# Performance work log

Hardware: AMD Instinct MI355X
Metric: run time of the kernel (lower is better)

Reference implementation:

```python
import jax, jax.numpy as jnp
import numpy as np

B, T, E, H = 2, 2048, 1024, 16


def setup_inputs() -> dict:
    key = jax.random.key(0)
    ks = jax.random.split(key, 6)
    s = lambda k, shape: jax.random.normal(k, shape, dtype=jnp.float32) * 0.02
    return {
        "x": jax.random.normal(ks[0], (B, T, E), dtype=jnp.float32),
        "ln1_g": jnp.ones((E,), jnp.float32),
        "ln1_b": jnp.zeros((E,), jnp.float32),
        "attn_w": s(ks[1], (E, 3 * E)),
        "attn_b": jnp.zeros((3 * E,), jnp.float32),
        "proj_w": s(ks[2], (E, E)),
        "proj_b": jnp.zeros((E,), jnp.float32),
        "ln2_g": jnp.ones((E,), jnp.float32),
        "ln2_b": jnp.zeros((E,), jnp.float32),
        "mlp_w1": s(ks[3], (E, 4 * E)),
        "mlp_b1": jnp.zeros((4 * E,), jnp.float32),
        "mlp_w2": s(ks[4], (4 * E, E)),
        "mlp_b2": jnp.zeros((E,), jnp.float32),
        "w_att": jnp.ones((1,), jnp.float32),
        "w_mlp": jnp.ones((1,), jnp.float32),
    }


def _ln(x, g, b, eps=1e-5):
    m = x.mean(-1, keepdims=True)
    v = ((x - m) ** 2).mean(-1, keepdims=True)
    return (x - m) * jax.lax.rsqrt(v + eps) * g + b


def reference(x, ln1_g, ln1_b, attn_w, attn_b, proj_w, proj_b,
              ln2_g, ln2_b, mlp_w1, mlp_b1, mlp_w2, mlp_b2, w_att, w_mlp):
    Bx, Tx, Ex = x.shape
    hd = Ex // H
    # --- self-attention on ln_1(x) ---
    qkv = _ln(x, ln1_g, ln1_b) @ attn_w + attn_b          # [B,T,3E]
    q, k, v = jnp.split(qkv, 3, axis=-1)
    q = q.reshape(Bx, Tx, H, hd)
    k = k.reshape(Bx, Tx, H, hd)
    v = v.reshape(Bx, Tx, H, hd)
    att = jnp.einsum('bthd,bshd->bhts', q, k) * (1.0 / np.sqrt(hd))  # [B,H,T,T]
    causal = jnp.tril(jnp.ones((Tx, Tx), dtype=bool))
    att = jnp.where(causal, att, -jnp.inf)
    att = jax.nn.softmax(att, axis=-1)
    y = jnp.einsum('bhts,bshd->bthd', att, v).reshape(Bx, Tx, Ex)
    y = y @ proj_w + proj_b
    x = x * w_att + y
    # --- MLP on ln_2(x) ---
    h = _ln(x, ln2_g, ln2_b) @ mlp_w1 + mlp_b1
    h = jax.nn.gelu(h, approximate=False)
    x = x * w_mlp + (h @ mlp_w2 + mlp_b2)
    return x
```

## Files before the change

### kernel.cpp

```cpp
#include <hip/hip_runtime.h>
#include <math.h>

typedef __bf16 bf16;
typedef bf16 bf16x8 __attribute__((ext_vector_type(8)));
typedef bf16 bf16x4 __attribute__((ext_vector_type(4)));
typedef float f32x4 __attribute__((ext_vector_type(4)));

#define MFMA(a, b, c) __builtin_amdgcn_mfma_f32_16x16x32_bf16((a), (b), (c), 0, 0, 0)

#define GLOAD_LDS16(gp, lp)                                                        \
  __builtin_amdgcn_global_load_lds((const __attribute__((address_space(1))) void*)(gp), \
                                   (__attribute__((address_space(3))) void*)(lp), 16, 0, 0)

static const size_t E_WT_ATTN = 0;
static const size_t E_WT_PROJ = 3145728;
static const size_t E_WT_MLP1 = 4194304;
static const size_t E_WT_MLP2 = 8388608;
static const size_t E_LN1     = 12582912;
static const size_t E_QKV     = 16777216;
static const size_t E_VT      = 37748736;
static const size_t E_Y       = 41943040;
static const size_t E_LN2     = 46137344;
static const size_t E_H       = 50331648;
static const size_t BYTE_X2    = 134217728;
static const size_t BYTE_OPART = 150994944;
static const size_t BYTE_ML    = 184549376;
static const size_t BYTE_GPART = 185597952;
static const size_t TOTAL_BYTES = 252706816;

__device__ __align__(4096) unsigned char g_buf[TOTAL_BYTES];

__global__ __launch_bounds__(256) void transpose_cast(const float* __restrict__ in,
                                                      bf16* __restrict__ out, int K, int N) {
  __shared__ float tile[32][33];
  int bx = blockIdx.x, by = blockIdx.y;
  int tx = threadIdx.x, ty = threadIdx.y;
#pragma unroll
  for (int i = ty; i < 32; i += 8)
    tile[i][tx] = in[(size_t)(by * 32 + i) * N + bx * 32 + tx];
  __syncthreads();
#pragma unroll
  for (int i = ty; i < 32; i += 8)
    out[(size_t)(bx * 32 + i) * K + by * 32 + tx] = (bf16)tile[tx][i];
}

__global__ __launch_bounds__(256) void ln_bf16(const float* __restrict__ x,
                                               const float* __restrict__ g,
                                               const float* __restrict__ b,
                                               bf16* __restrict__ out) {
  int row = blockIdx.x, tid = threadIdx.x;
  const float* xr = x + ((size_t)row << 10);
  float4 v = *(const float4*)(xr + tid * 4);
  float s = v.x + v.y + v.z + v.w;
  float ss = v.x * v.x + v.y * v.y + v.z * v.z + v.w * v.w;
#pragma unroll
  for (int off = 32; off >= 1; off >>= 1) {
    s += __shfl_down(s, off);
    ss += __shfl_down(ss, off);
  }
  __shared__ float sh[8];
  int wid = tid >> 6;
  if ((tid & 63) == 0) { sh[wid] = s; sh[wid + 4] = ss; }
  __syncthreads();
  float ts = sh[0] + sh[1] + sh[2] + sh[3];
  float tss = sh[4] + sh[5] + sh[6] + sh[7];
  float mean = ts * (1.0f / 1024.0f);
  float var = tss * (1.0f / 1024.0f) - mean * mean;
  float inv = rsqrtf(var + 1e-5f);
  float4 gg = *(const float4*)(g + tid * 4);
  float4 bb = *(const float4*)(b + tid * 4);
  bf16x4 o;
  o[0] = (bf16)((v.x - mean) * inv * gg.x + bb.x);
  o[1] = (bf16)((v.y - mean) * inv * gg.y + bb.y);
  o[2] = (bf16)((v.z - mean) * inv * gg.z + bb.z);
  o[3] = (bf16)((v.w - mean) * inv * gg.w + bb.w);
  *(bf16x4*)(out + ((size_t)row << 10) + tid * 4) = o;
}

template <int EPI>
__global__ __launch_bounds__(512, 2) void gemm256(const bf16* __restrict__ A,
                                                  const bf16* __restrict__ Bt,
                                                  const float* __restrict__ bias,
                                                  bf16* __restrict__ outb,
                                                  float* __restrict__ outf,
                                                  int M, int N, int K, int Kseg) {
  __shared__ __align__(16) bf16 As[2][16384];
  __shared__ __align__(16) bf16 Bs[2][16384];
  int tid = threadIdx.x;
  int nwg = gridDim.x * gridDim.y;
  int bid = blockIdx.y * gridDim.x + blockIdx.x;
  int id2 = ((nwg & 7) == 0) ? ((bid & 7) * (nwg >> 3) + (bid >> 3)) : bid;
  int bx = id2 % gridDim.x, by = id2 / gridDim.x;
  int lane = tid & 63, wid = tid >> 6;
  int wr = wid >> 2, wc = wid & 3;
  int g = lane >> 4, lr = lane & 15;
  f32x4 acc[8][4];
#pragma unroll
  for (int m = 0; m < 8; ++m)
#pragma unroll
    for (int n = 0; n < 4; ++n) acc[m][n] = (f32x4){0.f, 0.f, 0.f, 0.f};
  const bf16* Ab = A + (size_t)by * 256 * K;
  const bf16* Bb = Bt + (size_t)bx * 256 * K;
  int rbase = tid >> 3;
  int srccol = (((tid & 7) ^ (rbase & 7)) << 3);
  const bf16* Asrc = Ab + (size_t)rbase * K + srccol;
  const bf16* Bsrc = Bb + (size_t)rbase * K + srccol;
#define G256_STAGE(buf, k0)                                                \
  {                                                                        \
    _Pragma("unroll") for (int q = 0; q < 4; ++q) {                        \
      GLOAD_LDS16(Asrc + (size_t)(q * 64) * K + (k0), &As[buf][tid * 8 + q * 4096]); \
      GLOAD_LDS16(Bsrc + (size_t)(q * 64) * K + (k0), &Bs[buf][tid * 8 + q * 4096]); \
    }                                                                      \
  }
  int kbeg = blockIdx.z * Kseg;
  int NT = Kseg >> 6;
  G256_STAGE(0, kbeg);
  __syncthreads();
  int c = 0;
  for (int t = 0; t < NT; ++t) {
    if (t + 1 < NT) G256_STAGE(c ^ 1, kbeg + (t + 1) * 64);
#pragma unroll
    for (int kk = 0; kk < 2; ++kk) {
      bf16x8 af[8], bfv[4];
#pragma unroll
      for (int m = 0; m < 8; ++m) {
        int row = wr * 128 + m * 16 + lr;
        af[m] = *(const bf16x8*)&As[c][row * 64 + ((((kk << 2) + g) ^ (row & 7)) << 3)];
      }
#pragma unroll
      for (int n = 0; n < 4; ++n) {
        int row = wc * 64 + n * 16 + lr;
        bfv[n] = *(const bf16x8*)&Bs[c][row * 64 + ((((kk << 2) + g) ^ (row & 7)) << 3)];
      }
#pragma unroll
      for (int m = 0; m < 8; ++m)
#pragma unroll
        for (int n = 0; n < 4; ++n) acc[m][n] = MFMA(af[m], bfv[n], acc[m][n]);
    }
    __syncthreads();
    c ^= 1;
  }
#undef G256_STAGE
  if (EPI == 3) {
    float* po = outf + (size_t)blockIdx.z * M * N;
#pragma unroll
    for (int m = 0; m < 8; ++m) {
#pragma unroll
      for (int n = 0; n < 4; ++n) {
        int rg0 = by * 256 + wr * 128 + m * 16 + g * 4;
        int cg = bx * 256 + wc * 64 + n * 16 + lr;
#pragma unroll
        for (int j = 0; j < 4; ++j) po[(size_t)(rg0 + j) * N + cg] = acc[m][n][j];
      }
    }
  } else {
#pragma unroll
    for (int m = 0; m < 8; ++m) {
#pragma unroll
      for (int n = 0; n < 4; ++n) {
        int rg0 = by * 256 + wr * 128 + m * 16 + g * 4;
        int cg = bx * 256 + wc * 64 + n * 16 + lr;
        float bv = bias[cg];
#pragma unroll
        for (int j = 0; j < 4; ++j) {
          float v = acc[m][n][j] + bv;
          size_t idx = (size_t)(rg0 + j) * N + cg;
          if (EPI == 0)
            outb[idx] = (bf16)v;
          else
            outb[idx] = (bf16)(0.5f * v * (1.0f + erff(v * 0.70710678118f)));
        }
      }
    }
  }
}

__global__ __launch_bounds__(256) void gemm_bt3(const bf16* __restrict__ A,
                                                const bf16* __restrict__ Bt,
                                                float* __restrict__ outf,
                                                int M, int N, int K, int Kseg) {
  __shared__ __align__(16) bf16 As[128 * 32];
  __shared__ __align__(16) bf16 Bs[128 * 32];
  int bx = blockIdx.x, by = blockIdx.y;
  int tid = threadIdx.x;
  int lane = tid & 63, wid = tid >> 6;
  int wr = wid >> 1, wc = wid & 1;
  int g = lane >> 4, lr = lane & 15;
  f32x4 acc[4][4];
#pragma unroll
  for (int m = 0; m < 4; ++m)
#pragma unroll
    for (int n = 0; n < 4; ++n) acc[m][n] = (f32x4){0.f, 0.f, 0.f, 0.f};
  const bf16* Ab = A + (size_t)by * 128 * K;
  const bf16* Bb = Bt + (size_t)bx * 128 * K;
  int srow = tid >> 2;
  int sk8 = (tid & 3) * 8;
  const bf16* Ap0 = Ab + (size_t)srow * K + sk8;
  const bf16* Ap1 = Ab + (size_t)(srow + 64) * K + sk8;
  const bf16* Bp0 = Bb + (size_t)srow * K + sk8;
  const bf16* Bp1 = Bb + (size_t)(srow + 64) * K + sk8;
  bf16* lA0 = As + tid * 8;
  bf16* lA1 = As + 2048 + tid * 8;
  bf16* lB0 = Bs + tid * 8;
  bf16* lB1 = Bs + 2048 + tid * 8;
  int kbeg = blockIdx.z * Kseg;
  int kend = kbeg + Kseg;
  for (int k0 = kbeg; k0 < kend; k0 += 32) {
    GLOAD_LDS16(Ap0 + k0, lA0);
    GLOAD_LDS16(Ap1 + k0, lA1);
    GLOAD_LDS16(Bp0 + k0, lB0);
    GLOAD_LDS16(Bp1 + k0, lB1);
    __syncthreads();
    bf16x8 af[4], bfv[4];
#pragma unroll
    for (int m = 0; m < 4; ++m) af[m] = *(const bf16x8*)(As + (wr * 64 + m * 16 + lr) * 32 + g * 8);
#pragma unroll
    for (int n = 0; n < 4; ++n) bfv[n] = *(const bf16x8*)(Bs + (wc * 64 + n * 16 + lr) * 32 + g * 8);
#pragma unroll
    for (int m = 0; m < 4; ++m)
#pragma unroll
      for (int n = 0; n < 4; ++n) acc[m][n] = MFMA(af[m], bfv[n], acc[m][n]);
    __syncthreads();
  }
  float* po = outf + (size_t)blockIdx.z * M * N;
#pragma unroll
  for (int m = 0; m < 4; ++m) {
#pragma unroll
    for (int n = 0; n < 4; ++n) {
      int rg0 = by * 128 + wr * 64 + m * 16 + g * 4;
      int cg = bx * 128 + wc * 64 + n * 16 + lr;
#pragma unroll
      for (int j = 0; j < 4; ++j) po[(size_t)(rg0 + j) * N + cg] = acc[m][n][j];
    }
  }
}

template <int SK>
__global__ __launch_bounds__(256) void reduce_add(const float* __restrict__ part,
                                                  const float* __restrict__ bias,
                                                  const float* __restrict__ res,
                                                  const float* __restrict__ wsc,
                                                  float* __restrict__ out, int MN, int N) {
  size_t i = ((size_t)blockIdx.x * 256 + threadIdx.x) * 4;
  float4 a = *(const float4*)(part + i);
#pragma unroll
  for (int s = 1; s < SK; ++s) {
    float4 b = *(const float4*)(part + (size_t)s * MN + i);
    a.x += b.x; a.y += b.y; a.z += b.z; a.w += b.w;
  }
  int col = (int)(i & (size_t)(N - 1));
  float4 bv = *(const float4*)(bias + col);
  float4 rv = *(const float4*)(res + i);
  float w = wsc[0];
  float4 o;
  o.x = rv.x * w + a.x + bv.x;
  o.y = rv.y * w + a.y + bv.y;
  o.z = rv.z * w + a.z + bv.z;
  o.w = rv.w * w + a.w + bv.w;
  *(float4*)(out + i) = o;
}

__global__ __launch_bounds__(256) void reduce_ln(const float* __restrict__ part,
                                                 const float* __restrict__ bias,
                                                 const float* __restrict__ res,
                                                 const float* __restrict__ wsc,
                                                 const float* __restrict__ lng,
                                                 const float* __restrict__ lnb,
                                                 float* __restrict__ x2out,
                                                 bf16* __restrict__ lnout) {
  int row = blockIdx.x, tid = threadIdx.x;
  size_t i = ((size_t)row << 10) + tid * 4;
  float4 a = *(const float4*)(part + i);
  float4 b2 = *(const float4*)(part + 4194304 + i);
  float4 rv = *(const float4*)(res + i);
  float4 bv = *(const float4*)(bias + tid * 4);
  float w = wsc[0];
  float4 o;
  o.x = rv.x * w + a.x + b2.x + bv.x;
  o.y = rv.y * w + a.y + b2.y + bv.y;
  o.z = rv.z * w + a.z + b2.z + bv.z;
  o.w = rv.w * w + a.w + b2.w + bv.w;
  *(float4*)(x2out + i) = o;
  float s = o.x + o.y + o.z + o.w;
  float ss = o.x * o.x + o.y * o.y + o.z * o.z + o.w * o.w;
#pragma unroll
  for (int off = 32; off >= 1; off >>= 1) {
    s += __shfl_down(s, off);
    ss += __shfl_down(ss, off);
  }
  __shared__ float sh[8];
  int wid = tid >> 6;
  if ((tid & 63) == 0) { sh[wid] = s; sh[wid + 4] = ss; }
  __syncthreads();
  float ts = sh[0] + sh[1] + sh[2] + sh[3];
  float tss = sh[4] + sh[5] + sh[6] + sh[7];
  float mean = ts * (1.0f / 1024.0f);
  float var = tss * (1.0f / 1024.0f) - mean * mean;
  float inv = rsqrtf(var + 1e-5f);
  float4 gg = *(const float4*)(lng + tid * 4);
  float4 bb = *(const float4*)(lnb + tid * 4);
  bf16x4 ov;
  ov[0] = (bf16)((o.x - mean) * inv * gg.x + bb.x);
  ov[1] = (bf16)((o.y - mean) * inv * gg.y + bb.y);
  ov[2] = (bf16)((o.z - mean) * inv * gg.z + bb.z);
  ov[3] = (bf16)((o.w - mean) * inv * gg.w + bb.w);
  *(bf16x4*)(lnout + ((size_t)row << 10) + tid * 4) = ov;
}

__global__ __launch_bounds__(256) void split_v_t(const bf16* __restrict__ qkv,
                                                 bf16* __restrict__ vT) {
  int t0 = blockIdx.x * 32;
  int bh = blockIdx.y;
  int b = bh >> 4, h = bh & 15;
  __shared__ bf16 tile[32][72];
  int tid = threadIdx.x;
  int d = tid & 63, tl0 = tid >> 6;
#pragma unroll
  for (int p = 0; p < 8; ++p) {
    int tl = p * 4 + tl0;
    tile[tl][d] = qkv[((size_t)(b * 2048 + t0 + tl)) * 3072 + 2048 + h * 64 + d];
  }
  __syncthreads();
  int tl = tid & 31, dq = tid >> 5;
#pragma unroll
  for (int p = 0; p < 8; ++p) {
    int dd = p * 8 + dq;
    vT[((size_t)(bh * 64 + dd)) * 2048 + t0 + tl] = tile[tl][dd];
  }
}

__global__ __launch_bounds__(256) void attn_fwd(const bf16* __restrict__ qkv,
                                                const bf16* __restrict__ vT,
                                                float* __restrict__ o_part,
                                                float* __restrict__ ml_part) {
  __shared__ __align__(16) bf16 Ks[2][4096];
  __shared__ __align__(16) bf16 Vs[2][4096];
  __shared__ bf16 P[4][16][72];
  int id = blockIdx.x;
  int bh = id & 31;
  int seg = (id >> 5) & 1;
  int qi = ((id >> 6) + bh) & 31;
  int tid = threadIdx.x, wid = tid >> 6, lane = tid & 63;
  int g = lane >> 4, lr = lane & 15;
  int b = bh >> 4, h = bh & 15;
  int nk = qi + 1;
  int n0 = (nk + 1) >> 1;
  int kt0 = seg ? n0 : 0;
  int kt1 = seg ? nk : n0;
  int qrow = qi * 64 + wid * 16 + lr;
  const bf16* Qr = qkv + ((size_t)(b * 2048 + qrow)) * 3072 + h * 64;
  bf16x8 qf[2];
  qf[0] = *(const bf16x8*)(Qr + g * 8);
  qf[1] = *(const bf16x8*)(Qr + 32 + g * 8);
  int r0 = tid >> 3, cs0 = ((tid & 7) ^ (r0 & 7)) << 3;
  int c1i = tid + 256;
  int r1 = c1i >> 3, cs1 = ((c1i & 7) ^ (r1 & 7)) << 3;
  const bf16* sK0 = qkv + ((size_t)(b * 2048 + r0)) * 3072 + 1024 + h * 64 + cs0;
  const bf16* sK1 = qkv + ((size_t)(b * 2048 + r1)) * 3072 + 1024 + h * 64 + cs1;
  const bf16* sV0 = vT + (size_t)bh * 131072 + (size_t)r0 * 2048 + cs0;
  const bf16* sV1 = vT + (size_t)bh * 131072 + (size_t)r1 * 2048 + cs1;
  bf16* dK0 = &Ks[0][0] + tid * 8;
  bf16* dK1 = &Ks[0][0] + 2048 + tid * 8;
  bf16* dV0 = &Vs[0][0] + tid * 8;
  bf16* dV1 = &Vs[0][0] + 2048 + tid * 8;
#define ATTN_STAGE(bufsel, ktv)                          \
  {                                                      \
    size_t kadv = (size_t)(ktv) * (64 * 3072);           \
    size_t vadv = (size_t)(ktv) * 64;                    \
    int bo = (bufsel) * 4096;                            \
    GLOAD_LDS16(sK0 + kadv, dK0 + bo);                   \
    GLOAD_LDS16(sK1 + kadv, dK1 + bo);                   \
    GLOAD_LDS16(sV0 + vadv, dV0 + bo);                   \
    GLOAD_LDS16(sV1 + vadv, dV1 + bo);                   \
  }
  f32x4 o[4];
#pragma unroll
  for (int n = 0; n < 4; ++n) o[n] = (f32x4){0.f, 0.f, 0.f, 0.f};
  float m = -3e38f, l = 0.f;
  if (kt0 < kt1) ATTN_STAGE(0, kt0);
  __syncthreads();
  const float beta = 0.18033688f;
  int sw = lr & 7;
  int sb = (lane & 48) | (g << 2);
  for (int kt = kt0; kt < kt1; ++kt) {
    int cur = (kt - kt0) & 1;
    if (kt + 1 < kt1) ATTN_STAGE(cur ^ 1, kt + 1);
    const bf16* Kb = &Ks[cur][0];
    const bf16* Vb = &Vs[cur][0];
    f32x4 s[4];
#pragma unroll
    for (int n = 0; n < 4; ++n) s[n] = (f32x4){0.f, 0.f, 0.f, 0.f};
#pragma unroll
    for (int kk = 0; kk < 2; ++kk) {
#pragma unroll
      for (int n = 0; n < 4; ++n) {
        bf16x8 kf = *(const bf16x8*)(Kb + ((n * 16 + lr) << 6) + ((((kk << 2) + g) ^ sw) << 3));
        s[n] = MFMA(kf, qf[kk], s[n]);
      }
    }
    int kc0 = kt * 64 + g * 4;
#pragma unroll
    for (int n = 0; n < 4; ++n)
#pragma unroll
      for (int j = 0; j < 4; ++j) {
        float sv = s[n][j] * beta;
        s[n][j] = ((kc0 + n * 16 + j) <= qrow) ? sv : -3e38f;
      }
    float mx = s[0][0];
#pragma unroll
    for (int n = 0; n < 4; ++n)
#pragma unroll
      for (int j = 0; j < 4; ++j) mx = fmaxf(mx, s[n][j]);
    mx = fmaxf(mx, __shfl_xor(mx, 16));
    mx = fmaxf(mx, __shfl_xor(mx, 32));
    float mn = fmaxf(m, mx);
    float al = exp2f(m - mn);
    m = mn;
    float rs = 0.f;
    bf16x4 pw[4];
#pragma unroll
    for (int n = 0; n < 4; ++n)
#pragma unroll
      for (int j = 0; j < 4; ++j) {
        float p = exp2f(s[n][j] - mn);
        rs += p;
        pw[n][j] = (bf16)p;
      }
    rs += __shfl_xor(rs, 16);
    rs += __shfl_xor(rs, 32);
    l = l * al + rs;
    float alj[4];
#pragma unroll
    for (int j = 0; j < 4; ++j) alj[j] = __shfl(al, sb + j);
#pragma unroll
    for (int n = 0; n < 4; ++n)
#pragma unroll
      for (int j = 0; j < 4; ++j) o[n][j] *= alj[j];
#pragma unroll
    for (int n = 0; n < 4; ++n) *(bf16x4*)&P[wid][lr][n * 16 + g * 4] = pw[n];
#pragma unroll
    for (int kk = 0; kk < 2; ++kk) {
      bf16x8 pf = *(const bf16x8*)&P[wid][lr][kk * 32 + g * 8];
#pragma unroll
      for (int n = 0; n < 4; ++n) {
        bf16x8 vf = *(const bf16x8*)(Vb + ((n * 16 + lr) << 6) + ((((kk << 2) + g) ^ sw) << 3));
        o[n] = MFMA(pf, vf, o[n]);
      }
    }
    __syncthreads();
  }
  float* ob = o_part + (size_t)id * 4096;
#pragma unroll
  for (int n = 0; n < 4; ++n)
#pragma unroll
    for (int j = 0; j < 4; ++j)
      ob[(size_t)(wid * 16 + g * 4 + j) * 64 + n * 16 + lr] = o[n][j];
  if (lane < 16) {
    ml_part[(size_t)id * 128 + (wid * 16 + lane) * 2] = m;
    ml_part[(size_t)id * 128 + (wid * 16 + lane) * 2 + 1] = l;
  }
#undef ATTN_STAGE
}

__global__ __launch_bounds__(256) void attn_combine(const float* __restrict__ o_part,
                                                    const float* __restrict__ ml_part,
                                                    bf16* __restrict__ y) {
  int c = blockIdx.x;
  int bh = c & 31, qi = c >> 5;
  int b = bh >> 4, h = bh & 15;
  int qraw = (qi - bh) & 31;
  size_t id0 = (size_t)bh + ((size_t)qraw << 6);
  size_t id1 = id0 + 32;
  int t = threadIdx.x;
  int r = t >> 2, cq = (t & 3) << 4;
  float m1 = ml_part[id0 * 128 + r * 2], l1 = ml_part[id0 * 128 + r * 2 + 1];
  float m2 = ml_part[id1 * 128 + r * 2], l2 = ml_part[id1 * 128 + r * 2 + 1];
  float mm = fmaxf(m1, m2);
  float w1 = exp2f(m1 - mm), w2 = exp2f(m2 - mm);
  float inv = 1.0f / (l1 * w1 + l2 * w2);
  const float* p1 = o_part + id0 * 4096 + r * 64 + cq;
  const float* p2 = o_part + id1 * 4096 + r * 64 + cq;
  bf16* yp = y + ((size_t)(b * 2048 + qi * 64 + r)) * 1024 + h * 64 + cq;
#pragma unroll
  for (int u = 0; u < 4; ++u) {
    float4 a = *(const float4*)(p1 + u * 4);
    float4 bq = *(const float4*)(p2 + u * 4);
    bf16x4 ov;
    ov[0] = (bf16)((a.x * w1 + bq.x * w2) * inv);
    ov[1] = (bf16)((a.y * w1 + bq.y * w2) * inv);
    ov[2] = (bf16)((a.z * w1 + bq.z * w2) * inv);
    ov[3] = (bf16)((a.w * w1 + bq.w * w2) * inv);
    *(bf16x4*)(yp + u * 4) = ov;
  }
}

extern "C" void kernel_launch(void* const* d_in, const int* in_sizes, int n_in,
                              void* d_out, int out_size, void* d_ws, size_t ws_size,
                              hipStream_t stream) {
  const float* x = (const float*)d_in[0];
  const float* ln1_g = (const float*)d_in[1];
  const float* ln1_b = (const float*)d_in[2];
  const float* attn_w = (const float*)d_in[3];
  const float* attn_b = (const float*)d_in[4];
  const float* proj_w = (const float*)d_in[5];
  const float* proj_b = (const float*)d_in[6];
  const float* ln2_g = (const float*)d_in[7];
  const float* ln2_b = (const float*)d_in[8];
  const float* mlp_w1 = (const float*)d_in[9];
  const float* mlp_b1 = (const float*)d_in[10];
  const float* mlp_w2 = (const float*)d_in[11];
  const float* mlp_b2 = (const float*)d_in[12];
  const float* w_att = (const float*)d_in[13];
  const float* w_mlp = (const float*)d_in[14];
  float* out = (float*)d_out;

  unsigned char* base = nullptr;
  if (ws_size >= TOTAL_BYTES) {
    base = (unsigned char*)d_ws;
  } else {
    hipGetSymbolAddress((void**)&base, HIP_SYMBOL(g_buf));
  }
  bf16* bb = (bf16*)base;
  bf16* wt_attn = bb + E_WT_ATTN;
  bf16* wt_proj = bb + E_WT_PROJ;
  bf16* wt_mlp1 = bb + E_WT_MLP1;
  bf16* wt_mlp2 = bb + E_WT_MLP2;
  bf16* ln1o = bb + E_LN1;
  bf16* qkv = bb + E_QKV;
  bf16* vTb = bb + E_VT;
  bf16* yb = bb + E_Y;
  bf16* ln2o = bb + E_LN2;
  bf16* hb = bb + E_H;
  float* x2 = (float*)(base + BYTE_X2);
  float* o_part = (float*)(base + BYTE_OPART);
  float* ml_part = (float*)(base + BYTE_ML);
  float* gpart = (float*)(base + BYTE_GPART);

  dim3 tb(32, 8);
  transpose_cast<<<dim3(3072 / 32, 1024 / 32), tb, 0, stream>>>(attn_w, wt_attn, 1024, 3072);
  transpose_cast<<<dim3(1024 / 32, 1024 / 32), tb, 0, stream>>>(proj_w, wt_proj, 1024, 1024);
  transpose_cast<<<dim3(4096 / 32, 1024 / 32), tb, 0, stream>>>(mlp_w1, wt_mlp1, 1024, 4096);
  transpose_cast<<<dim3(1024 / 32, 4096 / 32), tb, 0, stream>>>(mlp_w2, wt_mlp2, 4096, 1024);

  ln_bf16<<<4096, 256, 0, stream>>>(x, ln1_g, ln1_b, ln1o);

  gemm256<0><<<dim3(12, 16, 1), 512, 0, stream>>>(ln1o, wt_attn, attn_b, qkv, nullptr,
                                                  4096, 3072, 1024, 1024);

  split_v_t<<<dim3(64, 32), 256, 0, stream>>>(qkv, vTb);

  attn_fwd<<<2048, 256, 0, stream>>>(qkv, vTb, o_part, ml_part);
  attn_combine<<<1024, 256, 0, stream>>>(o_part, ml_part, yb);

  gemm_bt3<<<dim3(8, 32, 2), 256, 0, stream>>>(yb, wt_proj, gpart, 4096, 1024, 1024, 512);
  reduce_ln<<<4096, 256, 0, stream>>>(gpart, proj_b, x, w_att, ln2_g, ln2_b, x2, ln2o);

  gemm256<1><<<dim3(16, 16, 1), 512, 0, stream>>>(ln2o, wt_mlp1, mlp_b1, hb, nullptr,
                                                  4096, 4096, 1024, 1024);

  gemm256<3><<<dim3(4, 16, 4), 512, 0, stream>>>(hb, wt_mlp2, nullptr, nullptr, gpart,
                                                 4096, 1024, 4096, 1024);
  reduce_add<4><<<4096, 256, 0, stream>>>(gpart, mlp_b2, x2, w_mlp, out, 4194304, 1024);
}
```

Baseline: 404.0 us.

## Merge weight transposes, use tanh GELU, fold Q scale, skip masking, defer rescale

Merges the four weight transpose-cast launches into one grid that picks its matrix from the block index. Replaces the erf GELU with the tanh approximation built from exp2f. In attention, Q is pre-scaled by the softmax constant, the causal mask is applied only on the diagonal tile, and the running-max rescale of the output accumulator is skipped when the new max stays within a threshold. The tanh GELU changes numerics relative to the exact erf reference, and the deferred rescale lets unnormalized exponentials grow before bf16 rounding.

```diff
diff --git a/kernel.cpp b/kernel.cpp
--- a/kernel.cpp
+++ b/kernel.cpp
@@ -30,10 +30,25 @@
 
 __device__ __align__(4096) unsigned char g_buf[TOTAL_BYTES];
 
-__global__ __launch_bounds__(256) void transpose_cast(const float* __restrict__ in,
-                                                      bf16* __restrict__ out, int K, int N) {
+__global__ __launch_bounds__(256) void transpose_all(const float* __restrict__ aw,
+                                                     const float* __restrict__ pw,
+                                                     const float* __restrict__ m1,
+                                                     const float* __restrict__ m2,
+                                                     bf16* __restrict__ o_a,
+                                                     bf16* __restrict__ o_p,
+                                                     bf16* __restrict__ o_m1,
+                                                     bf16* __restrict__ o_m2) {
   __shared__ float tile[32][33];
-  int bx = blockIdx.x, by = blockIdx.y;
+  int bid = blockIdx.x;
+  const float* in;
+  bf16* out;
+  int K, N, tix;
+  if (bid < 3072) { in = aw; out = o_a; K = 1024; N = 3072; tix = bid; }
+  else if (bid < 4096) { in = pw; out = o_p; K = 1024; N = 1024; tix = bid - 3072; }
+  else if (bid < 8192) { in = m1; out = o_m1; K = 1024; N = 4096; tix = bid - 4096; }
+  else { in = m2; out = o_m2; K = 4096; N = 1024; tix = bid - 8192; }
+  int ntx = N >> 5;
+  int bx = tix % ntx, by = tix / ntx;
   int tx = threadIdx.x, ty = threadIdx.y;
 #pragma unroll
   for (int i = ty; i < 32; i += 8)
@@ -167,8 +182,12 @@
           size_t idx = (size_t)(rg0 + j) * N + cg;
           if (EPI == 0)
             outb[idx] = (bf16)v;
-          else
-            outb[idx] = (bf16)(0.5f * v * (1.0f + erff(v * 0.70710678118f)));
+          else {
+            float u = 0.7978845608f * (v + 0.044715f * v * v * v);
+            float e = exp2f(u * 2.885390082f);
+            float th = 1.0f - 2.0f / (e + 1.0f);
+            outb[idx] = (bf16)(0.5f * v * (1.0f + th));
+          }
         }
       }
     }
@@ -349,9 +368,14 @@
   int kt1 = seg ? nk : n0;
   int qrow = qi * 64 + wid * 16 + lr;
   const bf16* Qr = qkv + ((size_t)(b * 2048 + qrow)) * 3072 + h * 64;
+  const float beta = 0.18033688f;
   bf16x8 qf[2];
   qf[0] = *(const bf16x8*)(Qr + g * 8);
   qf[1] = *(const bf16x8*)(Qr + 32 + g * 8);
+#pragma unroll
+  for (int kk = 0; kk < 2; ++kk)
+#pragma unroll
+    for (int e = 0; e < 8; ++e) qf[kk][e] = (bf16)((float)qf[kk][e] * beta);
   int r0 = tid >> 3, cs0 = ((tid & 7) ^ (r0 & 7)) << 3;
   int c1i = tid + 256;
   int r1 = c1i >> 3, cs1 = ((c1i & 7) ^ (r1 & 7)) << 3;
@@ -379,7 +403,6 @@
   float m = -3e38f, l = 0.f;
   if (kt0 < kt1) ATTN_STAGE(0, kt0);
   __syncthreads();
-  const float beta = 0.18033688f;
   int sw = lr & 7;
   int sb = (lane & 48) | (g << 2);
   for (int kt = kt0; kt < kt1; ++kt) {
@@ -398,14 +421,14 @@
         s[n] = MFMA(kf, qf[kk], s[n]);
       }
     }
-    int kc0 = kt * 64 + g * 4;
-#pragma unroll
-    for (int n = 0; n < 4; ++n)
-#pragma unroll
-      for (int j = 0; j < 4; ++j) {
-        float sv = s[n][j] * beta;
-        s[n][j] = ((kc0 + n * 16 + j) <= qrow) ? sv : -3e38f;
-      }
+    if (kt == qi) {
+      int kc0 = kt * 64 + g * 4;
+#pragma unroll
+      for (int n = 0; n < 4; ++n)
+#pragma unroll
+        for (int j = 0; j < 4; ++j)
+          if ((kc0 + n * 16 + j) > qrow) s[n][j] = -3e38f;
+    }
     float mx = s[0][0];
 #pragma unroll
     for (int n = 0; n < 4; ++n)
@@ -413,9 +436,13 @@
       for (int j = 0; j < 4; ++j) mx = fmaxf(mx, s[n][j]);
     mx = fmaxf(mx, __shfl_xor(mx, 16));
     mx = fmaxf(mx, __shfl_xor(mx, 32));
-    float mn = fmaxf(m, mx);
-    float al = exp2f(m - mn);
-    m = mn;
+    bool defer = __all(mx <= m + 11.5416f);
+    float mn = m, al = 0.f;
+    if (!defer) {
+      mn = fmaxf(m, mx);
+      al = exp2f(m - mn);
+      m = mn;
+    }
     float rs = 0.f;
     bf16x4 pw[4];
 #pragma unroll
@@ -428,14 +455,18 @@
       }
     rs += __shfl_xor(rs, 16);
     rs += __shfl_xor(rs, 32);
-    l = l * al + rs;
-    float alj[4];
-#pragma unroll
-    for (int j = 0; j < 4; ++j) alj[j] = __shfl(al, sb + j);
-#pragma unroll
-    for (int n = 0; n < 4; ++n)
-#pragma unroll
-      for (int j = 0; j < 4; ++j) o[n][j] *= alj[j];
+    if (defer) {
+      l += rs;
+    } else {
+      l = l * al + rs;
+      float alj[4];
+#pragma unroll
+      for (int j = 0; j < 4; ++j) alj[j] = __shfl(al, sb + j);
+#pragma unroll
+      for (int n = 0; n < 4; ++n)
+#pragma unroll
+        for (int j = 0; j < 4; ++j) o[n][j] *= alj[j];
+    }
 #pragma unroll
     for (int n = 0; n < 4; ++n) *(bf16x4*)&P[wid][lr][n * 16 + g * 4] = pw[n];
 #pragma unroll
@@ -536,11 +567,8 @@
   float* ml_part = (float*)(base + BYTE_ML);
   float* gpart = (float*)(base + BYTE_GPART);
 
-  dim3 tb(32, 8);
-  transpose_cast<<<dim3(3072 / 32, 1024 / 32), tb, 0, stream>>>(attn_w, wt_attn, 1024, 3072);
-  transpose_cast<<<dim3(1024 / 32, 1024 / 32), tb, 0, stream>>>(proj_w, wt_proj, 1024, 1024);
-  transpose_cast<<<dim3(4096 / 32, 1024 / 32), tb, 0, stream>>>(mlp_w1, wt_mlp1, 1024, 4096);
-  transpose_cast<<<dim3(1024 / 32, 4096 / 32), tb, 0, stream>>>(mlp_w2, wt_mlp2, 4096, 1024);
+  transpose_all<<<12288, dim3(32, 8), 0, stream>>>(attn_w, proj_w, mlp_w1, mlp_w2,
+                                                   wt_attn, wt_proj, wt_mlp1, wt_mlp2);
 
   ln_bf16<<<4096, 256, 0, stream>>>(x, ln1_g, ln1_b, ln1o);
 
```

Result: faster. 385.2 us (-4.6%).
